# Optimization experiments

Measured on AMD Instinct MI355X. Metric: run time of the kernel, lower is better.

## Reference

```python
import jax, jax.numpy as jnp
import numpy as np

N_NODES = 35
N_EDGES = 1190
N_VIEWS = 6
C1_IN, C1_OUT = 1, 256
C2_IN, C2_OUT = 256, 256
C3_IN, C3_OUT = 256, 64


def _nnconv(x, edge_attr, src, dst, nn_w, nn_b, lin_w, bias, c_in, c_out):
    """PyG NNConv with aggr='mean': per-edge MLP weight, gather-matvec-scatter."""
    # per-edge weight matrices: [E, c_in, c_out]
    W = jax.nn.relu(edge_attr @ nn_w.T + nn_b).reshape(-1, c_in, c_out)
    # gather source features and apply per-edge weight: [E, c_out]
    msg = jnp.einsum('ei,eio->eo', x[src], W)
    # scatter-mean into target nodes
    agg = jax.ops.segment_sum(msg, dst, num_segments=N_NODES)
    cnt = jax.ops.segment_sum(jnp.ones((msg.shape[0],), msg.dtype), dst,
                              num_segments=N_NODES)
    agg = agg / jnp.maximum(cnt, 1.0)[:, None]
    # root transform (lin has no bias in PyG) + conv bias
    return agg + x @ lin_w.T + bias


def setup_inputs() -> dict:
    key = jax.random.key(0)
    ks = jax.random.split(key, 16)
    s = 0.05
    x = jnp.ones((N_NODES, C1_IN), jnp.float32)
    edge_attr = jax.random.uniform(ks[0], (N_EDGES, N_VIEWS), jnp.float32)
    edge_index = jax.random.randint(ks[1], (2, N_EDGES), 0, N_NODES, jnp.int32)
    inp = {
        'x': x, 'edge_attr': edge_attr, 'edge_index': edge_index,
        'nn1_w': jax.random.normal(ks[2], (C1_IN * C1_OUT, N_VIEWS), jnp.float32) * s,
        'nn1_b': jax.random.normal(ks[3], (C1_IN * C1_OUT,), jnp.float32) * s,
        'lin1_w': jax.random.normal(ks[4], (C1_OUT, C1_IN), jnp.float32) * s,
        'b1': jax.random.normal(ks[5], (C1_OUT,), jnp.float32) * s,
        'nn2_w': jax.random.normal(ks[6], (C2_IN * C2_OUT, N_VIEWS), jnp.float32) * s,
        'nn2_b': jax.random.normal(ks[7], (C2_IN * C2_OUT,), jnp.float32) * s,
        'lin2_w': jax.random.normal(ks[8], (C2_OUT, C2_IN), jnp.float32) * s,
        'b2': jax.random.normal(ks[9], (C2_OUT,), jnp.float32) * s,
        'nn3_w': jax.random.normal(ks[10], (C3_IN * C3_OUT, N_VIEWS), jnp.float32) * s,
        'nn3_b': jax.random.normal(ks[11], (C3_IN * C3_OUT,), jnp.float32) * s,
        'lin3_w': jax.random.normal(ks[12], (C3_OUT, C3_IN), jnp.float32) * s,
        'b3': jax.random.normal(ks[13], (C3_OUT,), jnp.float32) * s,
    }
    return inp


def reference(x, edge_attr, edge_index, nn1_w, nn1_b, lin1_w, b1,
              nn2_w, nn2_b, lin2_w, b2, nn3_w, nn3_b, lin3_w, b3):
    src, dst = edge_index[0], edge_index[1]
    x = jax.nn.relu(_nnconv(x, edge_attr, src, dst, nn1_w, nn1_b, lin1_w, b1, C1_IN, C1_OUT))
    x = jax.nn.relu(_nnconv(x, edge_attr, src, dst, nn2_w, nn2_b, lin2_w, b2, C2_IN, C2_OUT))
    x = jax.nn.relu(_nnconv(x, edge_attr, src, dst, nn3_w, nn3_b, lin3_w, b3, C3_IN, C3_OUT))
    # CBT: pairwise L1 distances over feature dim -> [N, N]
    # (equivalent to repeat(35,1,1) / transpose / abs / sum since N == 35)
    cbt = jnp.abs(x[None, :, :] - x[:, None, :]).sum(-1)
    return cbt
```

## Files before the change

### kernel.cpp

```cpp
#include <hip/hip_runtime.h>


#define NN 35
#define NE 1190
#define TE 10
#define NG 119

#define OFF_AGG1 0
#define OFF_AGG2 8960
#define OFF_AGG3 17920
#define OFF_CNT  20160
#define ZERO_N   20195
#define OFF_L2T  20224
#define OFF_X2M  85760
#define OFF_X3   94720

__global__ __launch_bounds__(256) void prep_k(float* __restrict__ ws,
                                              const float* __restrict__ lin2) {
    int b = blockIdx.x, t = threadIdx.x;
    if (b < 80) {
        int idx = b * 256 + t;
        if (idx < ZERO_N) ws[idx] = 0.f;
    } else {
        int i = b - 80;
        ws[OFF_L2T + i * 256 + t] = lin2[t * 256 + i];
    }
}

__global__ __launch_bounds__(512) void msg1_k(
    const float* __restrict__ x, const float* __restrict__ ea,
    const int* __restrict__ ei, const float* __restrict__ w1,
    const float* __restrict__ b1w, float* __restrict__ agg1,
    float* __restrict__ cnt) {
    int tid = threadIdx.x;
    int e = blockIdx.x * 2 + (tid >> 8);
    int o = tid & 255;
    int src = ei[e];
    int dst = ei[NE + e];
    float xs = x[src];
    const float* eap = ea + e * 6;
    const float* w = w1 + o * 6;
    float d = b1w[o];
#pragma unroll
    for (int v = 0; v < 6; v++) d = fmaf(eap[v], w[v], d);
    atomicAdd(agg1 + dst * 256 + o, xs * fmaxf(d, 0.f));
    if (o == 0) atomicAdd(cnt + dst, 1.0f);
}

__global__ __launch_bounds__(512, 4) void msg2x1_k(
    const float* __restrict__ x, const float* __restrict__ ea,
    const int* __restrict__ ei, const float* __restrict__ lin1,
    const float* __restrict__ b1, const float* __restrict__ agg1,
    const float* __restrict__ cnt, const float* __restrict__ w2,
    const float* __restrict__ b2w, float* __restrict__ agg2) {
    __shared__ float xs[TE][256];
    __shared__ float eas[TE][6];
    __shared__ int srcs[TE], dsts[TE];
    __shared__ float part[7][TE][64];
    int tid = threadIdx.x;
    int eg = blockIdx.x >> 2, og = blockIdx.x & 3;
    int e0 = eg * TE;
    if (tid < TE) { srcs[tid] = ei[e0 + tid]; dsts[tid] = ei[NE + e0 + tid]; }
    if (tid >= 64 && tid < 64 + TE * 6) {
        int t = tid - 64;
        eas[t / 6][t % 6] = ea[e0 * 6 + t];
    }
    __syncthreads();
    for (int idx = tid; idx < TE * 256; idx += 512) {
        int te = idx >> 8, i = idx & 255;
        int s = srcs[te];
        float c = fmaxf(cnt[s], 1.f);
        float v = agg1[s * 256 + i] / c + x[s] * lin1[i] + b1[i];
        xs[te][i] = fmaxf(v, 0.f);
    }
    __syncthreads();
    int ol = tid & 63;
    int o = og * 64 + ol;
    int ic = tid >> 6;
    float eareg[TE][6];
#pragma unroll
    for (int te = 0; te < TE; te++)
#pragma unroll
        for (int v = 0; v < 6; v++) eareg[te][v] = eas[te][v];
    float acc[TE] = {};
    for (int ii = 0; ii < 32; ii++) {
        int i = ic * 32 + ii;
        const float* w = w2 + (size_t)(i * 256 + o) * 6;
        float2 wa = *(const float2*)w;
        float2 wb = *(const float2*)(w + 2);
        float2 wc = *(const float2*)(w + 4);
        float b = b2w[i * 256 + o];
#pragma unroll
        for (int te = 0; te < TE; te += 2) {
            float dx = b, dy = b;
            dx = fmaf(eareg[te][0], wa.x, dx); dy = fmaf(eareg[te + 1][0], wa.x, dy);
            dx = fmaf(eareg[te][1], wa.y, dx); dy = fmaf(eareg[te + 1][1], wa.y, dy);
            dx = fmaf(eareg[te][2], wb.x, dx); dy = fmaf(eareg[te + 1][2], wb.x, dy);
            dx = fmaf(eareg[te][3], wb.y, dx); dy = fmaf(eareg[te + 1][3], wb.y, dy);
            dx = fmaf(eareg[te][4], wc.x, dx); dy = fmaf(eareg[te + 1][4], wc.x, dy);
            dx = fmaf(eareg[te][5], wc.y, dx); dy = fmaf(eareg[te + 1][5], wc.y, dy);
            dx = fmaxf(dx, 0.f);               dy = fmaxf(dy, 0.f);
            acc[te] = fmaf(xs[te][i], dx, acc[te]);
            acc[te + 1] = fmaf(xs[te + 1][i], dy, acc[te + 1]);
        }
    }
    if (ic > 0) {
#pragma unroll
        for (int te = 0; te < TE; te++) part[ic - 1][te][ol] = acc[te];
    }
    __syncthreads();
    if (ic == 0) {
#pragma unroll
        for (int te = 0; te < TE; te++) {
            float s = acc[te];
#pragma unroll
            for (int p = 0; p < 7; p++) s += part[p][te][ol];
            atomicAdd(agg2 + dsts[te] * 256 + o, s);
        }
    }
}

__global__ __launch_bounds__(512, 4) void msg3x2_k(
    const float* __restrict__ x, const float* __restrict__ ea,
    const int* __restrict__ ei, const float* __restrict__ lin1,
    const float* __restrict__ b1, const float* __restrict__ agg1,
    const float* __restrict__ cnt, const float* __restrict__ lin2T,
    const float* __restrict__ b2, const float* __restrict__ agg2,
    const float* __restrict__ w3, const float* __restrict__ b3w,
    float* __restrict__ agg3, float* __restrict__ x2m) {
    __shared__ float x1r[TE][256];
    __shared__ float xs[TE][64];
    __shared__ float eas[TE][6];
    __shared__ int srcs[TE], dsts[TE];
    __shared__ float part[7][TE][64];
    int tid = threadIdx.x;

    if (blockIdx.x >= 476) {
        int n = blockIdx.x - 476;
        float c = fmaxf(cnt[n], 1.f);
        if (tid < 256) {
            float v = agg1[n * 256 + tid] / c + x[n] * lin1[tid] + b1[tid];
            x1r[0][tid] = fmaxf(v, 0.f);
        }
        __syncthreads();
        int o = tid & 255, ic = tid >> 8;
        float s = 0.f;
        for (int ii = 0; ii < 128; ii++) {
            int i = ic * 128 + ii;
            s = fmaf(lin2T[i * 256 + o], x1r[0][i], s);
        }
        float* p2 = &part[0][0][0];
        if (ic == 1) p2[o] = s;
        __syncthreads();
        if (ic == 0) {
            float v = agg2[n * 256 + o] / c + s + p2[o] + b2[o];
            x2m[n * 256 + o] = fmaxf(v, 0.f);
        }
        return;
    }

    int eg = blockIdx.x >> 2, ig = blockIdx.x & 3;
    int e0 = eg * TE;
    if (tid < TE) { srcs[tid] = ei[e0 + tid]; dsts[tid] = ei[NE + e0 + tid]; }
    if (tid >= 64 && tid < 64 + TE * 6) {
        int t = tid - 64;
        eas[t / 6][t % 6] = ea[e0 * 6 + t];
    }
    __syncthreads();
    for (int idx = tid; idx < TE * 256; idx += 512) {
        int te = idx >> 8, i = idx & 255;
        int s = srcs[te];
        float c = fmaxf(cnt[s], 1.f);
        float v = agg1[s * 256 + i] / c + x[s] * lin1[i] + b1[i];
        x1r[te][i] = fmaxf(v, 0.f);
    }
    __syncthreads();
    int ol = tid & 63;
    int ic = tid >> 6;
    int o2 = ig * 64 + ol;
    {
        float acc2[TE] = {};
        for (int ii = 0; ii < 32; ii++) {
            int i = ic * 32 + ii;
            float w = lin2T[i * 256 + o2];
#pragma unroll
            for (int te = 0; te < TE; te++)
                acc2[te] = fmaf(w, x1r[te][i], acc2[te]);
        }
        if (ic > 0) {
#pragma unroll
            for (int te = 0; te < TE; te++) part[ic - 1][te][ol] = acc2[te];
        }
        __syncthreads();
        if (ic == 0) {
#pragma unroll
            for (int te = 0; te < TE; te++) {
                float ssum = acc2[te];
#pragma unroll
                for (int p = 0; p < 7; p++) ssum += part[p][te][ol];
                int s = srcs[te];
                float c = fmaxf(cnt[s], 1.f);
                float v = agg2[s * 256 + o2] / c + ssum + b2[o2];
                xs[te][ol] = fmaxf(v, 0.f);
            }
        }
        __syncthreads();
    }
    float eareg[TE][6];
#pragma unroll
    for (int te = 0; te < TE; te++)
#pragma unroll
        for (int v = 0; v < 6; v++) eareg[te][v] = eas[te][v];
    float acc[TE] = {};
    for (int jj = 0; jj < 8; jj++) {
        int ii = ic * 8 + jj;
        int i = ig * 64 + ii;
        const float* w = w3 + (size_t)(i * 64 + ol) * 6;
        float2 wa = *(const float2*)w;
        float2 wb = *(const float2*)(w + 2);
        float2 wc = *(const float2*)(w + 4);
        float b = b3w[i * 64 + ol];
#pragma unroll
        for (int te = 0; te < TE; te += 2) {
            float dx = b, dy = b;
            dx = fmaf(eareg[te][0], wa.x, dx); dy = fmaf(eareg[te + 1][0], wa.x, dy);
            dx = fmaf(eareg[te][1], wa.y, dx); dy = fmaf(eareg[te + 1][1], wa.y, dy);
            dx = fmaf(eareg[te][2], wb.x, dx); dy = fmaf(eareg[te + 1][2], wb.x, dy);
            dx = fmaf(eareg[te][3], wb.y, dx); dy = fmaf(eareg[te + 1][3], wb.y, dy);
            dx = fmaf(eareg[te][4], wc.x, dx); dy = fmaf(eareg[te + 1][4], wc.x, dy);
            dx = fmaf(eareg[te][5], wc.y, dx); dy = fmaf(eareg[te + 1][5], wc.y, dy);
            dx = fmaxf(dx, 0.f);               dy = fmaxf(dy, 0.f);
            acc[te] = fmaf(xs[te][ii], dx, acc[te]);
            acc[te + 1] = fmaf(xs[te + 1][ii], dy, acc[te + 1]);
        }
    }
    if (ic > 0) {
#pragma unroll
        for (int te = 0; te < TE; te++) part[ic - 1][te][ol] = acc[te];
    }
    __syncthreads();
    if (ic == 0) {
#pragma unroll
        for (int te = 0; te < TE; te++) {
            float s = acc[te];
#pragma unroll
            for (int p = 0; p < 7; p++) s += part[p][te][ol];
            atomicAdd(agg3 + dsts[te] * 64 + ol, s);
        }
    }
}

__global__ __launch_bounds__(256) void x3_k(
    const float* __restrict__ x2m, const float* __restrict__ lin3,
    const float* __restrict__ b3, const float* __restrict__ agg3,
    const float* __restrict__ cnt, float* __restrict__ x3) {
    __shared__ float xr[256];
    __shared__ float part[3][64];
    int n = blockIdx.x, tid = threadIdx.x;
    int o = tid & 63, ic = tid >> 6;
    xr[tid] = x2m[n * 256 + tid];
    __syncthreads();
    const float4* w = (const float4*)(lin3 + (size_t)o * 256 + ic * 64);
    float s = 0.f;
#pragma unroll
    for (int k = 0; k < 16; k++) {
        float4 wv = w[k];
        int i = ic * 64 + k * 4;
        s = fmaf(wv.x, xr[i], s);
        s = fmaf(wv.y, xr[i + 1], s);
        s = fmaf(wv.z, xr[i + 2], s);
        s = fmaf(wv.w, xr[i + 3], s);
    }
    if (ic > 0) part[ic - 1][o] = s;
    __syncthreads();
    if (ic == 0) {
        float tot = s + part[0][o] + part[1][o] + part[2][o];
        float c = fmaxf(cnt[n], 1.f);
        x3[n * 64 + o] = fmaxf(agg3[n * 64 + o] / c + tot + b3[o], 0.f);
    }
}

__global__ __launch_bounds__(256) void cbt_k(const float* __restrict__ x3,
                                             float* __restrict__ out) {
    int t = blockIdx.x * 256 + threadIdx.x;
    if (t >= NN * NN) return;
    int i = t / NN, j = t % NN;
    const float* a = x3 + i * 64;
    const float* b = x3 + j * 64;
    float s = 0.f;
#pragma unroll
    for (int f = 0; f < 64; f++) s += fabsf(a[f] - b[f]);
    out[t] = s;
}

extern "C" void kernel_launch(void* const* d_in, const int* in_sizes, int n_in,
                              void* d_out, int out_size, void* d_ws, size_t ws_size,
                              hipStream_t stream) {
    const float* x    = (const float*)d_in[0];
    const float* ea   = (const float*)d_in[1];
    const int*   ei   = (const int*)d_in[2];
    const float* nn1w = (const float*)d_in[3];
    const float* nn1b = (const float*)d_in[4];
    const float* lin1 = (const float*)d_in[5];
    const float* b1   = (const float*)d_in[6];
    const float* nn2w = (const float*)d_in[7];
    const float* nn2b = (const float*)d_in[8];
    const float* lin2 = (const float*)d_in[9];
    const float* b2   = (const float*)d_in[10];
    const float* nn3w = (const float*)d_in[11];
    const float* nn3b = (const float*)d_in[12];
    const float* lin3 = (const float*)d_in[13];
    const float* b3   = (const float*)d_in[14];

    float* ws    = (float*)d_ws;
    float* agg1  = ws + OFF_AGG1;
    float* agg2  = ws + OFF_AGG2;
    float* agg3  = ws + OFF_AGG3;
    float* cnt   = ws + OFF_CNT;
    float* lin2T = ws + OFF_L2T;
    float* x2m   = ws + OFF_X2M;
    float* x3v   = ws + OFF_X3;
    float* out   = (float*)d_out;

    prep_k<<<336, 256, 0, stream>>>(ws, lin2);
    msg1_k<<<NE / 2, 512, 0, stream>>>(x, ea, ei, nn1w, nn1b, agg1, cnt);
    msg2x1_k<<<NG * 4, 512, 0, stream>>>(x, ea, ei, lin1, b1, agg1, cnt,
                                         nn2w, nn2b, agg2);
    msg3x2_k<<<NG * 4 + NN, 512, 0, stream>>>(x, ea, ei, lin1, b1, agg1, cnt,
                                              lin2T, b2, agg2, nn3w, nn3b,
                                              agg3, x2m);
    x3_k<<<NN, 256, 0, stream>>>(x2m, lin3, b3, agg3, cnt, x3v);
    cbt_k<<<(NN * NN + 255) / 256, 256, 0, stream>>>(x3v, out);
}
```

Before: 140.0 us.

## Fuse all stages into one cooperative persistent kernel with grid syncs

Replaces the chain of six kernel launches with a single cooperative kernel of 256 blocks that runs each stage in sequence, separated by grid-wide barriers. Work units of each stage are distributed over blocks with grid-stride loops. The aim is to remove per-launch overhead and inter-kernel gaps, which matter for this tiny graph workload. In exchange, only 256 blocks execute the larger stages, and each grid barrier has its own cost. The old multi-kernel path is kept as a fallback if the cooperative launch fails.

```diff
diff --git a/kernel.cpp b/kernel.cpp
--- a/kernel.cpp
+++ b/kernel.cpp
@@ -1,10 +1,18 @@
 #include <hip/hip_runtime.h>
+#include <hip/hip_cooperative_groups.h>
+
+namespace cg = cooperative_groups;
 
 
 #define NN 35
 #define NE 1190
 #define TE 10
 #define NG 119
+#define NU2 476
+#define NU3 511
+#define NB 256
+#define NT 512
+#define GSZ (NB * NT)
 
 #define OFF_AGG1 0
 #define OFF_AGG2 8960
@@ -14,6 +22,273 @@
 #define OFF_L2T  20224
 #define OFF_X2M  85760
 #define OFF_X3   94720
+
+__global__ __launch_bounds__(NT, 2) void mega_k(
+    const float* __restrict__ x, const float* __restrict__ ea,
+    const int* __restrict__ ei,
+    const float* __restrict__ w1, const float* __restrict__ b1w,
+    const float* __restrict__ lin1, const float* __restrict__ b1,
+    const float* __restrict__ w2, const float* __restrict__ b2w,
+    const float* __restrict__ lin2, const float* __restrict__ b2,
+    const float* __restrict__ w3, const float* __restrict__ b3w,
+    const float* __restrict__ lin3, const float* __restrict__ b3,
+    float* __restrict__ ws, float* __restrict__ out) {
+    cg::grid_group grid = cg::this_grid();
+    __shared__ float x1r[TE][256];
+    __shared__ float xs[TE][256];
+    __shared__ float eas[TE][6];
+    __shared__ int srcs[TE], dsts[TE];
+    __shared__ float part[7][TE][64];
+
+    float* agg1  = ws + OFF_AGG1;
+    float* agg2  = ws + OFF_AGG2;
+    float* agg3  = ws + OFF_AGG3;
+    float* cnt   = ws + OFF_CNT;
+    float* lin2T = ws + OFF_L2T;
+    float* x2m   = ws + OFF_X2M;
+    float* x3v   = ws + OFF_X3;
+
+    const int tid = threadIdx.x;
+    const int bid = blockIdx.x;
+    const int gtid = bid * NT + tid;
+    const int ol = tid & 63;
+    const int ic = tid >> 6;
+
+    for (int idx = gtid; idx < ZERO_N; idx += GSZ) ws[idx] = 0.f;
+    for (int idx = gtid; idx < 65536; idx += GSZ) {
+        int o = idx >> 8, i = idx & 255;
+        lin2T[i * 256 + o] = lin2[idx];
+    }
+    grid.sync();
+
+    for (int idx = gtid; idx < NE * 256; idx += GSZ) {
+        int e = idx >> 8, o = idx & 255;
+        int src = ei[e], dst = ei[NE + e];
+        const float* eap = ea + e * 6;
+        const float* w = w1 + o * 6;
+        float d = b1w[o];
+#pragma unroll
+        for (int v = 0; v < 6; v++) d = fmaf(eap[v], w[v], d);
+        atomicAdd(agg1 + dst * 256 + o, x[src] * fmaxf(d, 0.f));
+        if (o == 0) atomicAdd(cnt + dst, 1.f);
+    }
+    grid.sync();
+
+    for (int u = bid; u < NU2; u += NB) {
+        __syncthreads();
+        int eg = u >> 2, og = u & 3;
+        int e0 = eg * TE;
+        if (tid < TE) { srcs[tid] = ei[e0 + tid]; dsts[tid] = ei[NE + e0 + tid]; }
+        if (tid >= 64 && tid < 64 + TE * 6) {
+            int t = tid - 64;
+            eas[t / 6][t % 6] = ea[e0 * 6 + t];
+        }
+        __syncthreads();
+        for (int idx = tid; idx < TE * 256; idx += NT) {
+            int te = idx >> 8, i = idx & 255;
+            int s = srcs[te];
+            float c = fmaxf(cnt[s], 1.f);
+            float v = agg1[s * 256 + i] / c + x[s] * lin1[i] + b1[i];
+            xs[te][i] = fmaxf(v, 0.f);
+        }
+        __syncthreads();
+        int o = og * 64 + ol;
+        float eareg[TE][6];
+#pragma unroll
+        for (int te = 0; te < TE; te++)
+#pragma unroll
+            for (int v = 0; v < 6; v++) eareg[te][v] = eas[te][v];
+        float acc[TE] = {};
+        for (int ii = 0; ii < 32; ii++) {
+            int i = ic * 32 + ii;
+            const float* w = w2 + (size_t)(i * 256 + o) * 6;
+            float2 wa = *(const float2*)w;
+            float2 wb = *(const float2*)(w + 2);
+            float2 wc = *(const float2*)(w + 4);
+            float b = b2w[i * 256 + o];
+#pragma unroll
+            for (int te = 0; te < TE; te += 2) {
+                float dx = b, dy = b;
+                dx = fmaf(eareg[te][0], wa.x, dx); dy = fmaf(eareg[te + 1][0], wa.x, dy);
+                dx = fmaf(eareg[te][1], wa.y, dx); dy = fmaf(eareg[te + 1][1], wa.y, dy);
+                dx = fmaf(eareg[te][2], wb.x, dx); dy = fmaf(eareg[te + 1][2], wb.x, dy);
+                dx = fmaf(eareg[te][3], wb.y, dx); dy = fmaf(eareg[te + 1][3], wb.y, dy);
+                dx = fmaf(eareg[te][4], wc.x, dx); dy = fmaf(eareg[te + 1][4], wc.x, dy);
+                dx = fmaf(eareg[te][5], wc.y, dx); dy = fmaf(eareg[te + 1][5], wc.y, dy);
+                dx = fmaxf(dx, 0.f);               dy = fmaxf(dy, 0.f);
+                acc[te] = fmaf(xs[te][i], dx, acc[te]);
+                acc[te + 1] = fmaf(xs[te + 1][i], dy, acc[te + 1]);
+            }
+        }
+        if (ic > 0) {
+#pragma unroll
+            for (int te = 0; te < TE; te++) part[ic - 1][te][ol] = acc[te];
+        }
+        __syncthreads();
+        if (ic == 0) {
+#pragma unroll
+            for (int te = 0; te < TE; te++) {
+                float s = acc[te];
+#pragma unroll
+                for (int p = 0; p < 7; p++) s += part[p][te][ol];
+                atomicAdd(agg2 + dsts[te] * 256 + o, s);
+            }
+        }
+    }
+    grid.sync();
+
+    for (int u = bid; u < NU3; u += NB) {
+        __syncthreads();
+        if (u >= NU2) {
+            int n = u - NU2;
+            float c = fmaxf(cnt[n], 1.f);
+            if (tid < 256) {
+                float v = agg1[n * 256 + tid] / c + x[n] * lin1[tid] + b1[tid];
+                x1r[0][tid] = fmaxf(v, 0.f);
+            }
+            __syncthreads();
+            int o = tid & 255, icw = tid >> 8;
+            float s = 0.f;
+            for (int ii = 0; ii < 128; ii++) {
+                int i = icw * 128 + ii;
+                s = fmaf(lin2T[i * 256 + o], x1r[0][i], s);
+            }
+            float* p2 = &part[0][0][0];
+            if (icw == 1) p2[o] = s;
+            __syncthreads();
+            if (icw == 0) {
+                float v = agg2[n * 256 + o] / c + s + p2[o] + b2[o];
+                x2m[n * 256 + o] = fmaxf(v, 0.f);
+            }
+            continue;
+        }
+        int eg = u >> 2, ig = u & 3;
+        int e0 = eg * TE;
+        if (tid < TE) { srcs[tid] = ei[e0 + tid]; dsts[tid] = ei[NE + e0 + tid]; }
+        if (tid >= 64 && tid < 64 + TE * 6) {
+            int t = tid - 64;
+            eas[t / 6][t % 6] = ea[e0 * 6 + t];
+        }
+        __syncthreads();
+        for (int idx = tid; idx < TE * 256; idx += NT) {
+            int te = idx >> 8, i = idx & 255;
+            int s = srcs[te];
+            float c = fmaxf(cnt[s], 1.f);
+            float v = agg1[s * 256 + i] / c + x[s] * lin1[i] + b1[i];
+            x1r[te][i] = fmaxf(v, 0.f);
+        }
+        __syncthreads();
+        int o2 = ig * 64 + ol;
+        {
+            float acc2[TE] = {};
+            for (int ii = 0; ii < 32; ii++) {
+                int i = ic * 32 + ii;
+                float w = lin2T[i * 256 + o2];
+#pragma unroll
+                for (int te = 0; te < TE; te++)
+                    acc2[te] = fmaf(w, x1r[te][i], acc2[te]);
+            }
+            if (ic > 0) {
+#pragma unroll
+                for (int te = 0; te < TE; te++) part[ic - 1][te][ol] = acc2[te];
+            }
+            __syncthreads();
+            if (ic == 0) {
+#pragma unroll
+                for (int te = 0; te < TE; te++) {
+                    float ssum = acc2[te];
+#pragma unroll
+                    for (int p = 0; p < 7; p++) ssum += part[p][te][ol];
+                    int s = srcs[te];
+                    float c = fmaxf(cnt[s], 1.f);
+                    float v = agg2[s * 256 + o2] / c + ssum + b2[o2];
+                    xs[te][ol] = fmaxf(v, 0.f);
+                }
+            }
+            __syncthreads();
+        }
+        float eareg[TE][6];
+#pragma unroll
+        for (int te = 0; te < TE; te++)
+#pragma unroll
+            for (int v = 0; v < 6; v++) eareg[te][v] = eas[te][v];
+        float acc[TE] = {};
+        for (int jj = 0; jj < 8; jj++) {
+            int ii = ic * 8 + jj;
+            int i = ig * 64 + ii;
+            const float* w = w3 + (size_t)(i * 64 + ol) * 6;
+            float2 wa = *(const float2*)w;
+            float2 wb = *(const float2*)(w + 2);
+            float2 wc = *(const float2*)(w + 4);
+            float b = b3w[i * 64 + ol];
+#pragma unroll
+            for (int te = 0; te < TE; te += 2) {
+                float dx = b, dy = b;
+                dx = fmaf(eareg[te][0], wa.x, dx); dy = fmaf(eareg[te + 1][0], wa.x, dy);
+                dx = fmaf(eareg[te][1], wa.y, dx); dy = fmaf(eareg[te + 1][1], wa.y, dy);
+                dx = fmaf(eareg[te][2], wb.x, dx); dy = fmaf(eareg[te + 1][2], wb.x, dy);
+                dx = fmaf(eareg[te][3], wb.y, dx); dy = fmaf(eareg[te + 1][3], wb.y, dy);
+                dx = fmaf(eareg[te][4], wc.x, dx); dy = fmaf(eareg[te + 1][4], wc.x, dy);
+                dx = fmaf(eareg[te][5], wc.y, dx); dy = fmaf(eareg[te + 1][5], wc.y, dy);
+                dx = fmaxf(dx, 0.f);               dy = fmaxf(dy, 0.f);
+                acc[te] = fmaf(xs[te][ii], dx, acc[te]);
+                acc[te + 1] = fmaf(xs[te + 1][ii], dy, acc[te + 1]);
+            }
+        }
+        if (ic > 0) {
+#pragma unroll
+            for (int te = 0; te < TE; te++) part[ic - 1][te][ol] = acc[te];
+        }
+        __syncthreads();
+        if (ic == 0) {
+#pragma unroll
+            for (int te = 0; te < TE; te++) {
+                float s = acc[te];
+#pragma unroll
+                for (int p = 0; p < 7; p++) s += part[p][te][ol];
+                atomicAdd(agg3 + dsts[te] * 64 + ol, s);
+            }
+        }
+    }
+    grid.sync();
+
+    if (bid < NN) {
+        int n = bid;
+        if (tid < 256) x1r[0][tid] = x2m[n * 256 + tid];
+        __syncthreads();
+        const float4* w = (const float4*)(lin3 + (size_t)ol * 256 + ic * 32);
+        float s = 0.f;
+#pragma unroll
+        for (int k = 0; k < 8; k++) {
+            float4 wv = w[k];
+            int i = ic * 32 + k * 4;
+            s = fmaf(wv.x, x1r[0][i], s);
+            s = fmaf(wv.y, x1r[0][i + 1], s);
+            s = fmaf(wv.z, x1r[0][i + 2], s);
+            s = fmaf(wv.w, x1r[0][i + 3], s);
+        }
+        if (ic > 0) part[ic - 1][0][ol] = s;
+        __syncthreads();
+        if (ic == 0) {
+            float tot = s;
+#pragma unroll
+            for (int p = 0; p < 7; p++) tot += part[p][0][ol];
+            float c = fmaxf(cnt[n], 1.f);
+            x3v[n * 64 + ol] = fmaxf(agg3[n * 64 + ol] / c + tot + b3[ol], 0.f);
+        }
+    }
+    grid.sync();
+
+    for (int p = gtid; p < NN * NN; p += GSZ) {
+        int i = p / NN, j = p % NN;
+        const float* a = x3v + i * 64;
+        const float* bb = x3v + j * 64;
+        float s = 0.f;
+#pragma unroll
+        for (int f = 0; f < 64; f++) s += fabsf(a[f] - bb[f]);
+        out[p] = s;
+    }
+}
 
 __global__ __launch_bounds__(256) void prep_k(float* __restrict__ ws,
                                               const float* __restrict__ lin2) {
@@ -135,8 +410,8 @@
     __shared__ float part[7][TE][64];
     int tid = threadIdx.x;
 
-    if (blockIdx.x >= 476) {
-        int n = blockIdx.x - 476;
+    if (blockIdx.x >= NU2) {
+        int n = blockIdx.x - NU2;
         float c = fmaxf(cnt[n], 1.f);
         if (tid < 256) {
             float v = agg1[n * 256 + tid] / c + x[n] * lin1[tid] + b1[tid];
@@ -312,23 +587,33 @@
     const float* lin3 = (const float*)d_in[13];
     const float* b3   = (const float*)d_in[14];
 
-    float* ws    = (float*)d_ws;
-    float* agg1  = ws + OFF_AGG1;
-    float* agg2  = ws + OFF_AGG2;
-    float* agg3  = ws + OFF_AGG3;
-    float* cnt   = ws + OFF_CNT;
-    float* lin2T = ws + OFF_L2T;
-    float* x2m   = ws + OFF_X2M;
-    float* x3v   = ws + OFF_X3;
-    float* out   = (float*)d_out;
-
-    prep_k<<<336, 256, 0, stream>>>(ws, lin2);
-    msg1_k<<<NE / 2, 512, 0, stream>>>(x, ea, ei, nn1w, nn1b, agg1, cnt);
-    msg2x1_k<<<NG * 4, 512, 0, stream>>>(x, ea, ei, lin1, b1, agg1, cnt,
-                                         nn2w, nn2b, agg2);
-    msg3x2_k<<<NG * 4 + NN, 512, 0, stream>>>(x, ea, ei, lin1, b1, agg1, cnt,
-                                              lin2T, b2, agg2, nn3w, nn3b,
-                                              agg3, x2m);
-    x3_k<<<NN, 256, 0, stream>>>(x2m, lin3, b3, agg3, cnt, x3v);
-    cbt_k<<<(NN * NN + 255) / 256, 256, 0, stream>>>(x3v, out);
-}
+    float* ws  = (float*)d_ws;
+    float* out = (float*)d_out;
+
+    void* args[] = {
+        (void*)&x, (void*)&ea, (void*)&ei,
+        (void*)&nn1w, (void*)&nn1b, (void*)&lin1, (void*)&b1,
+        (void*)&nn2w, (void*)&nn2b, (void*)&lin2, (void*)&b2,
+        (void*)&nn3w, (void*)&nn3b, (void*)&lin3, (void*)&b3,
+        (void*)&ws, (void*)&out};
+    hipError_t err = hipLaunchCooperativeKernel(
+        (void*)mega_k, dim3(NB), dim3(NT), args, 0, stream);
+    if (err != hipSuccess) {
+        float* agg1  = ws + OFF_AGG1;
+        float* agg2  = ws + OFF_AGG2;
+        float* agg3  = ws + OFF_AGG3;
+        float* cnt   = ws + OFF_CNT;
+        float* lin2T = ws + OFF_L2T;
+        float* x2m   = ws + OFF_X2M;
+        float* x3v   = ws + OFF_X3;
+        prep_k<<<336, 256, 0, stream>>>(ws, lin2);
+        msg1_k<<<NE / 2, 512, 0, stream>>>(x, ea, ei, nn1w, nn1b, agg1, cnt);
+        msg2x1_k<<<NG * 4, 512, 0, stream>>>(x, ea, ei, lin1, b1, agg1, cnt,
+                                             nn2w, nn2b, agg2);
+        msg3x2_k<<<NG * 4 + NN, 512, 0, stream>>>(x, ea, ei, lin1, b1, agg1,
+                                                  cnt, lin2T, b2, agg2, nn3w,
+                                                  nn3b, agg3, x2m);
+        x3_k<<<NN, 256, 0, stream>>>(x2m, lin3, b3, agg3, cnt, x3v);
+        cbt_k<<<(NN * NN + 255) / 256, 256, 0, stream>>>(x3v, out);
+    }
+}
```

After: 312.2 us. 2.23x slower.

## Fuse x3 and CBT kernels, move weight transposes into msg1 kernel

Applied to the files above, without the earlier changes.

The lin2 transpose moves out of the zeroing prep kernel and, together with a new lin3 transpose, runs in extra blocks of the first message kernel. This leaves prep as a pure zero fill. The separate x3 and cbt kernels are merged into one kernel where every block recomputes all of x3 in shared memory and then writes one row of the distance matrix. This cuts one launch and a global round trip, but each of the 35 blocks repeats the full 35x64x256 lin3 product, so the final kernel does redundant work.

```diff
diff --git a/kernel.cpp b/kernel.cpp
--- a/kernel.cpp
+++ b/kernel.cpp
@@ -5,6 +5,7 @@
 #define NE 1190
 #define TE 10
 #define NG 119
+#define NU2 476
 
 #define OFF_AGG1 0
 #define OFF_AGG2 8960
@@ -13,26 +14,33 @@
 #define ZERO_N   20195
 #define OFF_L2T  20224
 #define OFF_X2M  85760
-#define OFF_X3   94720
-
-__global__ __launch_bounds__(256) void prep_k(float* __restrict__ ws,
-                                              const float* __restrict__ lin2) {
-    int b = blockIdx.x, t = threadIdx.x;
-    if (b < 80) {
-        int idx = b * 256 + t;
-        if (idx < ZERO_N) ws[idx] = 0.f;
-    } else {
-        int i = b - 80;
-        ws[OFF_L2T + i * 256 + t] = lin2[t * 256 + i];
-    }
-}
-
-__global__ __launch_bounds__(512) void msg1_k(
+#define OFF_L3T  94720
+
+__global__ __launch_bounds__(256) void prep_k(float* __restrict__ ws) {
+    int idx = blockIdx.x * 256 + threadIdx.x;
+    if (idx < ZERO_N) ws[idx] = 0.f;
+}
+
+__global__ __launch_bounds__(512) void msg1t_k(
     const float* __restrict__ x, const float* __restrict__ ea,
     const int* __restrict__ ei, const float* __restrict__ w1,
-    const float* __restrict__ b1w, float* __restrict__ agg1,
-    float* __restrict__ cnt) {
+    const float* __restrict__ b1w, const float* __restrict__ lin2,
+    const float* __restrict__ lin3, float* __restrict__ ws) {
     int tid = threadIdx.x;
+    if (blockIdx.x >= 595) {
+        int idx = (blockIdx.x - 595) * 512 + tid;
+        if (idx < 65536) {
+            int o = idx >> 8, i = idx & 255;
+            ws[OFF_L2T + i * 256 + o] = lin2[idx];
+        } else {
+            int idx2 = idx - 65536;
+            int o = idx2 >> 8, i = idx2 & 255;
+            ws[OFF_L3T + i * 64 + o] = lin3[idx2];
+        }
+        return;
+    }
+    float* agg1 = ws + OFF_AGG1;
+    float* cnt  = ws + OFF_CNT;
     int e = blockIdx.x * 2 + (tid >> 8);
     int o = tid & 255;
     int src = ei[e];
@@ -135,8 +143,8 @@
     __shared__ float part[7][TE][64];
     int tid = threadIdx.x;
 
-    if (blockIdx.x >= 476) {
-        int n = blockIdx.x - 476;
+    if (blockIdx.x >= NU2) {
+        int n = blockIdx.x - NU2;
         float c = fmaxf(cnt[n], 1.f);
         if (tid < 256) {
             float v = agg1[n * 256 + tid] / c + x[n] * lin1[tid] + b1[tid];
@@ -250,47 +258,36 @@
     }
 }
 
-__global__ __launch_bounds__(256) void x3_k(
-    const float* __restrict__ x2m, const float* __restrict__ lin3,
+__global__ __launch_bounds__(512) void x3cbt_k(
+    const float* __restrict__ x2m, const float* __restrict__ lin3T,
     const float* __restrict__ b3, const float* __restrict__ agg3,
-    const float* __restrict__ cnt, float* __restrict__ x3) {
-    __shared__ float xr[256];
-    __shared__ float part[3][64];
-    int n = blockIdx.x, tid = threadIdx.x;
-    int o = tid & 63, ic = tid >> 6;
-    xr[tid] = x2m[n * 256 + tid];
-    __syncthreads();
-    const float4* w = (const float4*)(lin3 + (size_t)o * 256 + ic * 64);
-    float s = 0.f;
-#pragma unroll
-    for (int k = 0; k < 16; k++) {
-        float4 wv = w[k];
-        int i = ic * 64 + k * 4;
-        s = fmaf(wv.x, xr[i], s);
-        s = fmaf(wv.y, xr[i + 1], s);
-        s = fmaf(wv.z, xr[i + 2], s);
-        s = fmaf(wv.w, xr[i + 3], s);
-    }
-    if (ic > 0) part[ic - 1][o] = s;
-    __syncthreads();
-    if (ic == 0) {
-        float tot = s + part[0][o] + part[1][o] + part[2][o];
+    const float* __restrict__ cnt, float* __restrict__ out) {
+    __shared__ float x2s[NN * 256];
+    __shared__ float x3s[NN * 65];
+    int tid = threadIdx.x;
+    for (int idx = tid; idx < NN * 256; idx += 512) x2s[idx] = x2m[idx];
+    __syncthreads();
+    for (int idx = tid; idx < NN * 64; idx += 512) {
+        int n = idx >> 6, o = idx & 63;
+        const float* xr = x2s + n * 256;
+        float s0 = 0.f, s1 = 0.f;
+        for (int i = 0; i < 256; i += 2) {
+            s0 = fmaf(lin3T[i * 64 + o], xr[i], s0);
+            s1 = fmaf(lin3T[(i + 1) * 64 + o], xr[i + 1], s1);
+        }
         float c = fmaxf(cnt[n], 1.f);
-        x3[n * 64 + o] = fmaxf(agg3[n * 64 + o] / c + tot + b3[o], 0.f);
-    }
-}
-
-__global__ __launch_bounds__(256) void cbt_k(const float* __restrict__ x3,
-                                             float* __restrict__ out) {
-    int t = blockIdx.x * 256 + threadIdx.x;
-    if (t >= NN * NN) return;
-    int i = t / NN, j = t % NN;
-    const float* a = x3 + i * 64;
-    const float* b = x3 + j * 64;
-    float s = 0.f;
-#pragma unroll
-    for (int f = 0; f < 64; f++) s += fabsf(a[f] - b[f]);
-    out[t] = s;
+        x3s[n * 65 + o] = fmaxf(agg3[idx] / c + s0 + s1 + b3[o], 0.f);
+    }
+    __syncthreads();
+    int i = blockIdx.x;
+    for (int j = tid; j < NN; j += 512) {
+        const float* a = x3s + i * 65;
+        const float* b = x3s + j * 65;
+        float s = 0.f;
+#pragma unroll
+        for (int f = 0; f < 64; f++) s += fabsf(a[f] - b[f]);
+        out[i * NN + j] = s;
+    }
 }
 
 extern "C" void kernel_launch(void* const* d_in, const int* in_sizes, int n_in,
@@ -319,16 +316,15 @@
     float* cnt   = ws + OFF_CNT;
     float* lin2T = ws + OFF_L2T;
     float* x2m   = ws + OFF_X2M;
-    float* x3v   = ws + OFF_X3;
+    float* lin3T = ws + OFF_L3T;
     float* out   = (float*)d_out;
 
-    prep_k<<<336, 256, 0, stream>>>(ws, lin2);
-    msg1_k<<<NE / 2, 512, 0, stream>>>(x, ea, ei, nn1w, nn1b, agg1, cnt);
+    prep_k<<<80, 256, 0, stream>>>(ws);
+    msg1t_k<<<755, 512, 0, stream>>>(x, ea, ei, nn1w, nn1b, lin2, lin3, ws);
     msg2x1_k<<<NG * 4, 512, 0, stream>>>(x, ea, ei, lin1, b1, agg1, cnt,
                                          nn2w, nn2b, agg2);
     msg3x2_k<<<NG * 4 + NN, 512, 0, stream>>>(x, ea, ei, lin1, b1, agg1, cnt,
                                               lin2T, b2, agg2, nn3w, nn3b,
                                               agg3, x2m);
-    x3_k<<<NN, 256, 0, stream>>>(x2m, lin3, b3, agg3, cnt, x3v);
-    cbt_k<<<(NN * NN + 255) / 256, 256, 0, stream>>>(x3v, out);
-}
+    x3cbt_k<<<NN, 512, 0, stream>>>(x2m, lin3T, b3, agg3, cnt, out);
+}
```

New measurement: 156.4 us. 11.7% more time.
